# Performance work log

Measured on AMD Instinct MI355X. Metric: run time of the kernel, lower is better.

Reference implementation:

```python
import jax, jax.numpy as jnp
import numpy as np

IMG = 128      # raster_settings.image_size
FOCAL = 1.5    # simple pinhole projection (camera transform)
EPS = 1e-8
B, V, F = 4, 600, 1000


def setup_inputs() -> dict:
    key = jax.random.key(0)
    k1, k2 = jax.random.split(key)
    u = jax.random.uniform(k1, (B, V, 3), dtype=jnp.float32)
    xy = u[..., :2] * 2.0 - 1.0          # x,y in [-1, 1]
    z = u[..., 2:3] * 2.0 + 1.0          # z in [1, 3] (in front of camera)
    verts = jnp.concatenate([xy, z], axis=-1)   # [B, V, 3] world coords
    faces = jax.random.randint(k2, (F, 3), 0, V)  # [F, 3] vertex indices
    return {"verts": verts, "faces": faces}


def _pix_grid(H, W):
    # PyTorch3D NDC convention: +X left, +Y up; pixel centers at (2i+1)/S - 1 flipped.
    xs = 1.0 - (2.0 * jnp.arange(W, dtype=jnp.float32) + 1.0) / W
    ys = 1.0 - (2.0 * jnp.arange(H, dtype=jnp.float32) + 1.0) / H
    px = jnp.broadcast_to(xs[None, :], (H, W)).reshape(-1)  # [P]
    py = jnp.broadcast_to(ys[:, None], (H, W)).reshape(-1)  # [P]
    return px, py


def _edge(ax, ay, bx, by, px, py):
    # signed (twice-)area of triangle (a, b, p)
    return (bx - ax) * (py - ay) - (by - ay) * (px - ax)


def _seg_dist2(px, py, ax, ay, bx, by):
    # squared distance from point p to segment (a, b); all args broadcastable
    ex, ey = bx - ax, by - ay
    dx, dy = px - ax, py - ay
    ee = jnp.maximum(ex * ex + ey * ey, EPS)
    t = jnp.clip((dx * ex + dy * ey) / ee, 0.0, 1.0)
    rx = dx - t * ex
    ry = dy - t * ey
    return rx * rx + ry * ry


def _rasterize_one(v_ndc, faces, H, W):
    fv = v_ndc[faces]                       # [F, 3, 3] face vertices (ndc x, y, view z)
    v0, v1, v2 = fv[:, 0], fv[:, 1], fv[:, 2]
    px, py = _pix_grid(H, W)                # [P], P = H*W
    pxr, pyr = px[None, :], py[None, :]
    # signed face area [F]
    area = _edge(v0[:, 0], v0[:, 1], v1[:, 0], v1[:, 1], v2[:, 0], v2[:, 1])
    # edge functions at every pixel -> unnormalized barycentrics [F, P]
    w0 = _edge(v1[:, 0:1], v1[:, 1:2], v2[:, 0:1], v2[:, 1:2], pxr, pyr)
    w1 = _edge(v2[:, 0:1], v2[:, 1:2], v0[:, 0:1], v0[:, 1:2], pxr, pyr)
    w2 = _edge(v0[:, 0:1], v0[:, 1:2], v1[:, 0:1], v1[:, 1:2], pxr, pyr)
    denom = jnp.where(jnp.abs(area) > EPS, area, EPS)[:, None]
    s0, s1, s2 = w0 / denom, w1 / denom, w2 / denom
    zpix = s0 * v0[:, 2:3] + s1 * v1[:, 2:3] + s2 * v2[:, 2:3]  # [F, P]
    inside = (s0 >= 0) & (s1 >= 0) & (s2 >= 0) \
             & (jnp.abs(area)[:, None] > EPS) & (zpix > 0)
    zcand = jnp.where(inside, zpix, jnp.inf)
    idx = jnp.argmin(zcand, axis=0)                       # [P] winning face per pixel
    gather = lambda a: jnp.take_along_axis(a, idx[None, :], axis=0)[0]
    zmin = gather(zcand)
    hit = jnp.isfinite(zmin)
    b0, b1, b2 = gather(s0), gather(s1), gather(s2)       # winner barycentrics [P]
    # signed squared point-triangle distance at the winning face (negative inside)
    fw = fv[idx]                                          # [P, 3, 3]
    a, b, c = fw[:, 0], fw[:, 1], fw[:, 2]
    d2 = jnp.minimum(
        jnp.minimum(_seg_dist2(px, py, a[:, 0], a[:, 1], b[:, 0], b[:, 1]),
                    _seg_dist2(px, py, b[:, 0], b[:, 1], c[:, 0], c[:, 1])),
        _seg_dist2(px, py, c[:, 0], c[:, 1], a[:, 0], a[:, 1]))
    pix_to_face = jnp.where(hit, idx, -1).reshape(H, W)
    zbuf = jnp.where(hit, zmin, -1.0).reshape(H, W)
    bary = jnp.where(hit[:, None], jnp.stack([b0, b1, b2], -1), -1.0).reshape(H, W, 3)
    dists = jnp.where(hit, -d2, -1.0).reshape(H, W)
    return pix_to_face, zbuf, bary, dists


def reference(verts, faces):
    # camera transform: identity world-to-view, perspective projection, keep view z
    x = FOCAL * verts[..., 0] / verts[..., 2]
    y = FOCAL * verts[..., 1] / verts[..., 2]
    v_ndc = jnp.stack([x, y, verts[..., 2]], axis=-1)     # [B, V, 3]
    rast = lambda v: _rasterize_one(v, faces, IMG, IMG)
    pix_to_face, zbuf, bary, dists = jax.vmap(rast)(v_ndc)
    return pix_to_face, zbuf, bary, dists
```

## Files before the change

kernel.cpp:

```cpp
#include <hip/hip_runtime.h>
#include <math.h>

namespace {

constexpr int IMG  = 128;
constexpr int NPIX = IMG * IMG;
constexpr int B    = 4;
constexpr int V    = 600;
constexpr int F    = 1000;
constexpr float FOCALF = 1.5f;
constexpr float EPSF   = 1e-8f;
constexpr float SLACK  = 1e-5f;
constexpr float ZEPS    = 1e-4f;
constexpr float DENSAFE = 1e-3f;

__device__ inline float seg_dist2(float px, float py, float ax, float ay,
                                  float bx, float by) {
#pragma clang fp contract(off)
    float ex = bx - ax, ey = by - ay;
    float dx = px - ax, dy = py - ay;
    float ee = fmaxf(ex * ex + ey * ey, EPSF);
    float t  = (dx * ex + dy * ey) / ee;
    t = fminf(fmaxf(t, 0.0f), 1.0f);
    float rx = dx - t * ex;
    float ry = dy - t * ey;
    return rx * rx + ry * ry;
}

__global__ __launch_bounds__(256) void setup_clear(const float* __restrict__ verts,
                                                   const int* __restrict__ faces,
                                                   float* __restrict__ fdata,
                                                   unsigned long long* __restrict__ zbest) {
#pragma clang fp contract(off)
    int t = blockIdx.x * 256 + threadIdx.x;
    zbest[t] = ~0ULL;
    if (t >= B * F) return;
    int b = t / F, f = t - b * F;
    int i0 = faces[f * 3 + 0], i1 = faces[f * 3 + 1], i2 = faces[f * 3 + 2];
    const float* vb = verts + (size_t)b * V * 3;
    float x0 = vb[i0 * 3], y0 = vb[i0 * 3 + 1], z0 = vb[i0 * 3 + 2];
    float x1 = vb[i1 * 3], y1 = vb[i1 * 3 + 1], z1 = vb[i1 * 3 + 2];
    float x2 = vb[i2 * 3], y2 = vb[i2 * 3 + 1], z2 = vb[i2 * 3 + 2];
    float ax = (FOCALF * x0) / z0, ay = (FOCALF * y0) / z0;
    float bx = (FOCALF * x1) / z1, by = (FOCALF * y1) / z1;
    float cx = (FOCALF * x2) / z2, cy = (FOCALF * y2) / z2;
    float e0x = cx - bx, e0y = cy - by;
    float e1x = ax - cx, e1y = ay - cy;
    float e2x = bx - ax, e2y = by - ay;
    float den = e2x * (cy - ay) - e2y * (cx - ax);
    if (!(fabsf(den) > EPSF)) den = 0.0f;
    float* o = fdata + ((size_t)t << 4);
    o[0]  = e0x; o[1]  = e0y; o[2]  = bx;  o[3]  = by;
    o[4]  = e1x; o[5]  = e1y; o[6]  = cx;  o[7]  = cy;
    o[8]  = e2x; o[9]  = e2y; o[10] = ax;  o[11] = ay;
    o[12] = den; o[13] = z0;  o[14] = z1;  o[15] = z2;
}

__global__ __launch_bounds__(512, 8) void rast(const float* __restrict__ fdata,
                                               unsigned long long* __restrict__ zbest) {
#pragma clang fp contract(off)
    __shared__ float4 sface[64 * 4];
    __shared__ unsigned int lticket;
    const int tid  = threadIdx.x;
    const int lane = tid & 63;
    const int bk   = blockIdx.x;
    const int ch   = bk & 15;
    const int b    = (bk >> 4) & 3;
    const int slice = bk >> 6;
    if (tid == 0) lticket = 0u;

    const int f0 = ch * 64;
    const int sz = min(64, F - f0);
    const int fl = min(f0 + lane, F - 1);
    const float4* fd4 = (const float4*)(fdata + (((size_t)b * F + fl) << 4));
    const float4 q0 = fd4[0], q1 = fd4[1], q2 = fd4[2], q3 = fd4[3];
    if (tid < 64) {
        sface[tid * 4 + 0] = q0;
        sface[tid * 4 + 1] = q1;
        sface[tid * 4 + 2] = q2;
        sface[tid * 4 + 3] = q3;
    }
    __syncthreads();

    const bool valid = (lane < sz) & (q3.x != 0.0f);
    const float s = q3.x > 0.0f ? 1.0f : -1.0f;
    const float g0x = s * q0.x, g0y = s * q0.y;
    const float g1x = s * q1.x, g1y = s * q1.y;
    const float g2x = s * q2.x, g2y = s * q2.y;
    const bool c0y = g0x >= 0.0f, c0x = g0y >= 0.0f;
    const bool c1y = g1x >= 0.0f, c1x = g1y >= 0.0f;
    const bool c2y = g2x >= 0.0f, c2x = g2y >= 0.0f;

    const int dpx = lane & 7, dpy = lane >> 3;

    for (;;) {
        unsigned int j = 0;
        if (lane == 0) j = atomicAdd(&lticket, 1u);
        j = (unsigned int)__shfl((int)j, 0);
        if (j >= 16u) break;
        const unsigned int jj = (j + (unsigned int)ch) & 15u;

        const int row = (slice >> 2) + 4 * (int)(jj >> 2);
        const int col = (slice & 3) + 4 * (int)(jj & 3);
        const int ix0 = col * 8, iy0 = row * 8;
        const int ix  = ix0 + dpx, iy = iy0 + dpy;
        const float px = 1.0f - (2.0f * (float)ix + 1.0f) / (float)IMG;
        const float py = 1.0f - (2.0f * (float)iy + 1.0f) / (float)IMG;
        const float pxmax = 1.0f - (2.0f * (float)ix0 + 1.0f) / (float)IMG;
        const float pxmin = 1.0f - (2.0f * (float)(ix0 + 7) + 1.0f) / (float)IMG;
        const float pymax = 1.0f - (2.0f * (float)iy0 + 1.0f) / (float)IMG;
        const float pymin = 1.0f - (2.0f * (float)(iy0 + 7) + 1.0f) / (float)IMG;

        const int gp = b * NPIX + iy * IMG + ix;
        const unsigned ztop = (unsigned)(zbest[gp] >> 32);
        float zbf  = (ztop == 0xFFFFFFFFu) ? INFINITY : __uint_as_float(ztop);
        float zbfp = zbf + ZEPS;

        bool pass = valid;
        pass &= (g0x * ((c0y ? pymax : pymin) - q0.w)
               - g0y * ((c0x ? pxmin : pxmax) - q0.z)) >= -SLACK;
        pass &= (g1x * ((c1y ? pymax : pymin) - q1.w)
               - g1y * ((c1x ? pxmin : pxmax) - q1.z)) >= -SLACK;
        pass &= (g2x * ((c2y ? pymax : pymin) - q2.w)
               - g2y * ((c2x ? pxmin : pxmax) - q2.z)) >= -SLACK;

        unsigned long long pmin = ~0ULL;
        unsigned long long mask = __ballot(pass);
        while (mask) {
            const int sl = __builtin_ctzll(mask);
            mask &= mask - 1;
            const float4 r0 = sface[sl * 4 + 0];
            const float4 r1 = sface[sl * 4 + 1];
            const float4 r2 = sface[sl * 4 + 2];
            const float4 r3 = sface[sl * 4 + 3];
            const float den = r3.x;
            float w0 = r0.x * (py - r0.w) - r0.y * (px - r0.z);
            float w1 = r1.x * (py - r1.w) - r1.y * (px - r1.z);
            float w2 = r2.x * (py - r2.w) - r2.y * (px - r2.z);

            const bool i0 = !(w0 * den < 0.0f);
            const bool i1 = !(w1 * den < 0.0f);
            const bool i2 = !(w2 * den < 0.0f);
            const float rd  = __builtin_amdgcn_rcpf(den);
            const float zt  = (w0 * rd) * r3.y + (w1 * rd) * r3.z + (w2 * rd) * r3.w;
            const bool densmall = fabsf(den) < DENSAFE;
            const bool need = (i0 & i1 & i2) &
                              (densmall | ((zt < zbfp) & (zt > -ZEPS)));
            if (__any(need)) {
                const unsigned ds = __float_as_uint(den) >> 31;
                const bool in0 = (w0 == 0.0f) | ((__float_as_uint(w0) >> 31) == ds);
                const bool in1 = (w1 == 0.0f) | ((__float_as_uint(w1) >> 31) == ds);
                const bool in2 = (w2 == 0.0f) | ((__float_as_uint(w2) >> 31) == ds);
                if (in0 & in1 & in2) {
                    float s0 = w0 / den, s1 = w1 / den, s2 = w2 / den;
                    float z  = s0 * r3.y + s1 * r3.z + s2 * r3.w;
                    if (z > 0.0f) {
                        unsigned long long pk =
                            ((unsigned long long)__float_as_uint(z) << 32) |
                            (unsigned)(f0 + sl);
                        pmin = pmin < pk ? pmin : pk;
                        zbf  = fminf(zbf, z);
                        zbfp = zbf + ZEPS;
                    }
                }
            }
        }
        if (pmin != ~0ULL) atomicMin(&zbest[gp], pmin);
    }
}

__global__ __launch_bounds__(256) void pass2(const float* __restrict__ fdata,
                                             const unsigned long long* __restrict__ zbest,
                                             float* __restrict__ out) {
#pragma clang fp contract(off)
    const int gp = blockIdx.x * 256 + threadIdx.x;
    const int b  = gp >> 14;
    const int p  = gp & (NPIX - 1);
    const int ix = p & (IMG - 1), iy = p >> 7;

    unsigned long long packed = zbest[gp];
    float o_face = -1.0f, o_z = -1.0f, o_b0 = -1.0f, o_b1 = -1.0f,
          o_b2 = -1.0f, o_d = -1.0f;

    if (packed != ~0ULL) {
        const int   idx = (int)(unsigned)(packed & 0xffffffffu);
        const float z   = __uint_as_float((unsigned)(packed >> 32));
        const float px  = 1.0f - (2.0f * (float)ix + 1.0f) / (float)IMG;
        const float py  = 1.0f - (2.0f * (float)iy + 1.0f) / (float)IMG;

        const float4* fd4 = (const float4*)(fdata + (((size_t)b * F + idx) << 4));
        float4 q0 = fd4[0], q1 = fd4[1], q2 = fd4[2], q3 = fd4[3];
        float den = q3.x;
        float w0 = q0.x * (py - q0.w) - q0.y * (px - q0.z);
        float w1 = q1.x * (py - q1.w) - q1.y * (px - q1.z);
        float w2 = q2.x * (py - q2.w) - q2.y * (px - q2.z);
        float s0 = w0 / den, s1 = w1 / den, s2 = w2 / den;

        float d2 = fminf(fminf(seg_dist2(px, py, q2.z, q2.w, q0.z, q0.w),
                               seg_dist2(px, py, q0.z, q0.w, q1.z, q1.w)),
                         seg_dist2(px, py, q1.z, q1.w, q2.z, q2.w));
        o_face = (float)idx; o_z = z;
        o_b0 = s0; o_b1 = s1; o_b2 = s2;
        o_d = -d2;
    }

    out[gp]            = o_face;
    out[B * NPIX + gp] = o_z;
    const int bary_base = 2 * B * NPIX;
    out[bary_base + gp * 3 + 0] = o_b0;
    out[bary_base + gp * 3 + 1] = o_b1;
    out[bary_base + gp * 3 + 2] = o_b2;
    out[5 * B * NPIX + gp] = o_d;
}

}

extern "C" void kernel_launch(void* const* d_in, const int* in_sizes, int n_in,
                              void* d_out, int out_size, void* d_ws, size_t ws_size,
                              hipStream_t stream) {
    const float* verts = (const float*)d_in[0];
    const int*   faces = (const int*)d_in[1];
    float* out = (float*)d_out;

    char* ws = (char*)d_ws;
    unsigned long long* zbest = (unsigned long long*)ws;
    float* fdata = (float*)(ws + (size_t)B * NPIX * 8);

    setup_clear<<<B * NPIX / 256, 256, 0, stream>>>(verts, faces, fdata, zbest);
    rast<<<1024, 512, 0, stream>>>(fdata, zbest);
    pass2<<<B * NPIX / 256, 256, 0, stream>>>(fdata, zbest, out);
}
```

Before: 31.78 us.

## Precompute normalized edge-function planes and z-plane for cheaper per-face culling

The face setup now precomputes sign-normalized edge equations (a*x+b*y+c), a barycentric sum constant, a linear depth plane, and a per-face depth tolerance. Face records grow from 16 to 28 floats and are padded to 1024 faces per batch, with degenerate or padding faces marked dead. The inner loop first runs a cheap two-FMA edge test with a wave-level early exit, then a planar depth test, and only loads the exact edge data for candidates. This cuts per-candidate ALU and LDS traffic in the hot loop, at the cost of more setup work and memory per face, plus new epsilon tolerances that could affect exactness.

```diff
diff --git a/kernel.cpp b/kernel.cpp
--- a/kernel.cpp
+++ b/kernel.cpp
@@ -8,10 +8,11 @@
 constexpr int B    = 4;
 constexpr int V    = 600;
 constexpr int F    = 1000;
+constexpr int FP   = 1024;
 constexpr float FOCALF = 1.5f;
 constexpr float EPSF   = 1e-8f;
-constexpr float SLACK  = 1e-5f;
-constexpr float ZEPS    = 1e-4f;
+constexpr float EW   = 1e-4f;
+constexpr float EBIN = 2e-4f;
 constexpr float DENSAFE = 1e-3f;
 
 __device__ inline float seg_dist2(float px, float py, float ax, float ay,
@@ -34,32 +35,59 @@
 #pragma clang fp contract(off)
     int t = blockIdx.x * 256 + threadIdx.x;
     zbest[t] = ~0ULL;
-    if (t >= B * F) return;
-    int b = t / F, f = t - b * F;
-    int i0 = faces[f * 3 + 0], i1 = faces[f * 3 + 1], i2 = faces[f * 3 + 2];
-    const float* vb = verts + (size_t)b * V * 3;
-    float x0 = vb[i0 * 3], y0 = vb[i0 * 3 + 1], z0 = vb[i0 * 3 + 2];
-    float x1 = vb[i1 * 3], y1 = vb[i1 * 3 + 1], z1 = vb[i1 * 3 + 2];
-    float x2 = vb[i2 * 3], y2 = vb[i2 * 3 + 1], z2 = vb[i2 * 3 + 2];
-    float ax = (FOCALF * x0) / z0, ay = (FOCALF * y0) / z0;
-    float bx = (FOCALF * x1) / z1, by = (FOCALF * y1) / z1;
-    float cx = (FOCALF * x2) / z2, cy = (FOCALF * y2) / z2;
-    float e0x = cx - bx, e0y = cy - by;
-    float e1x = ax - cx, e1y = ay - cy;
-    float e2x = bx - ax, e2y = by - ay;
-    float den = e2x * (cy - ay) - e2y * (cx - ax);
-    if (!(fabsf(den) > EPSF)) den = 0.0f;
-    float* o = fdata + ((size_t)t << 4);
-    o[0]  = e0x; o[1]  = e0y; o[2]  = bx;  o[3]  = by;
-    o[4]  = e1x; o[5]  = e1y; o[6]  = cx;  o[7]  = cy;
-    o[8]  = e2x; o[9]  = e2y; o[10] = ax;  o[11] = ay;
-    o[12] = den; o[13] = z0;  o[14] = z1;  o[15] = z2;
+    if (t >= B * FP) return;
+    const int b = t >> 10, fp = t & (FP - 1);
+    float* o = fdata + (size_t)t * 28;
+    bool dead = (fp >= F);
+    float e0x=0,e0y=0,bx=0,by=0,e1x=0,e1y=0,cx=0,cy=0,e2x=0,e2y=0,ax=0,ay=0;
+    float den=0, z0=0, z1=0, z2=0;
+    if (!dead) {
+        int i0 = faces[fp * 3 + 0], i1 = faces[fp * 3 + 1], i2 = faces[fp * 3 + 2];
+        const float* vb = verts + (size_t)b * V * 3;
+        float x0 = vb[i0 * 3], y0 = vb[i0 * 3 + 1]; z0 = vb[i0 * 3 + 2];
+        float x1 = vb[i1 * 3], y1 = vb[i1 * 3 + 1]; z1 = vb[i1 * 3 + 2];
+        float x2 = vb[i2 * 3], y2 = vb[i2 * 3 + 1]; z2 = vb[i2 * 3 + 2];
+        ax = (FOCALF * x0) / z0; ay = (FOCALF * y0) / z0;
+        bx = (FOCALF * x1) / z1; by = (FOCALF * y1) / z1;
+        cx = (FOCALF * x2) / z2; cy = (FOCALF * y2) / z2;
+        e0x = cx - bx; e0y = cy - by;
+        e1x = ax - cx; e1y = ay - cy;
+        e2x = bx - ax; e2y = by - ay;
+        den = e2x * (cy - ay) - e2y * (cx - ax);
+        if (!(fabsf(den) > EPSF)) { den = 0.0f; dead = true; }
+    }
+    if (dead) {
+        o[0] = 0.0f; o[1] = 0.0f; o[2] = -1e30f; o[3] = 0.0f;
+        #pragma unroll
+        for (int k = 4; k < 28; ++k) o[k] = 0.0f;
+        return;
+    }
+    float a0 = -e0y, b0 = e0x, c0 = e0y * bx - e0x * by;
+    float a1 = -e1y, b1 = e1x, c1 = e1y * cx - e1x * cy;
+    float a2 = -e2y, b2 = e2x, c2 = e2y * ax - e2x * ay;
+    const float s  = den > 0.0f ? 1.0f : -1.0f;
+    const float rd = __builtin_amdgcn_rcpf(den);
+    const float azr = z0 * rd, bzr = z1 * rd, czr = z2 * rd;
+    const float Zx = a0 * azr + a1 * bzr + a2 * czr;
+    const float Zy = b0 * azr + b1 * bzr + b2 * czr;
+    const float Zc = c0 * azr + c1 * bzr + c2 * czr;
+    const float S = (fabsf(a0) + fabsf(b0) + fabsf(c0)) * fabsf(azr)
+                  + (fabsf(a1) + fabsf(b1) + fabsf(c1)) * fabsf(bzr)
+                  + (fabsf(a2) + fabsf(b2) + fabsf(c2)) * fabsf(czr);
+    const float eps = (fabsf(den) < DENSAFE) ? INFINITY : (1e-4f + 2e-6f * S);
+    o[0]  = s * a0; o[1]  = s * b0; o[2]  = s * c0; o[3]  = s * den;
+    o[4]  = s * a1; o[5]  = s * b1; o[6]  = s * c1; o[7]  = eps;
+    o[8]  = Zx;     o[9]  = Zy;     o[10] = Zc;     o[11] = 0.0f;
+    o[12] = e0x;    o[13] = e0y;    o[14] = bx;     o[15] = by;
+    o[16] = e1x;    o[17] = e1y;    o[18] = cx;     o[19] = cy;
+    o[20] = e2x;    o[21] = e2y;    o[22] = ax;     o[23] = ay;
+    o[24] = den;    o[25] = z0;     o[26] = z1;     o[27] = z2;
 }
 
 __global__ __launch_bounds__(512, 8) void rast(const float* __restrict__ fdata,
                                                unsigned long long* __restrict__ zbest) {
 #pragma clang fp contract(off)
-    __shared__ float4 sface[64 * 4];
+    __shared__ float4 sface[64 * 7];
     __shared__ unsigned int lticket;
     const int tid  = threadIdx.x;
     const int lane = tid & 63;
@@ -70,26 +98,18 @@
     if (tid == 0) lticket = 0u;
 
     const int f0 = ch * 64;
-    const int sz = min(64, F - f0);
-    const int fl = min(f0 + lane, F - 1);
-    const float4* fd4 = (const float4*)(fdata + (((size_t)b * F + fl) << 4));
-    const float4 q0 = fd4[0], q1 = fd4[1], q2 = fd4[2], q3 = fd4[3];
-    if (tid < 64) {
-        sface[tid * 4 + 0] = q0;
-        sface[tid * 4 + 1] = q1;
-        sface[tid * 4 + 2] = q2;
-        sface[tid * 4 + 3] = q3;
-    }
+    const float4* gflat = (const float4*)(fdata + (size_t)(b * FP + f0) * 28);
+    if (tid < 448) ((float4*)sface)[tid] = gflat[tid];
+
+    const float4* fd4 = (const float4*)(fdata + (size_t)(b * FP + f0 + lane) * 28);
+    const float4 m0 = fd4[0], m1 = fd4[1];
+    const float a2s = -(m0.x + m1.x);
+    const float b2s = -(m0.y + m1.y);
+    const float c2s = m0.w - m0.z - m1.z;
+    const bool c0x = m0.x >= 0.0f, c0y = m0.y >= 0.0f;
+    const bool c1x = m1.x >= 0.0f, c1y = m1.y >= 0.0f;
+    const bool c2x = a2s >= 0.0f, c2y = b2s >= 0.0f;
     __syncthreads();
-
-    const bool valid = (lane < sz) & (q3.x != 0.0f);
-    const float s = q3.x > 0.0f ? 1.0f : -1.0f;
-    const float g0x = s * q0.x, g0y = s * q0.y;
-    const float g1x = s * q1.x, g1y = s * q1.y;
-    const float g2x = s * q2.x, g2y = s * q2.y;
-    const bool c0y = g0x >= 0.0f, c0x = g0y >= 0.0f;
-    const bool c1y = g1x >= 0.0f, c1x = g1y >= 0.0f;
-    const bool c2y = g2x >= 0.0f, c2x = g2y >= 0.0f;
 
     const int dpx = lane & 7, dpy = lane >> 3;
 
@@ -113,40 +133,42 @@
 
         const int gp = b * NPIX + iy * IMG + ix;
         const unsigned ztop = (unsigned)(zbest[gp] >> 32);
-        float zbf  = (ztop == 0xFFFFFFFFu) ? INFINITY : __uint_as_float(ztop);
-        float zbfp = zbf + ZEPS;
-
-        bool pass = valid;
-        pass &= (g0x * ((c0y ? pymax : pymin) - q0.w)
-               - g0y * ((c0x ? pxmin : pxmax) - q0.z)) >= -SLACK;
-        pass &= (g1x * ((c1y ? pymax : pymin) - q1.w)
-               - g1y * ((c1x ? pxmin : pxmax) - q1.z)) >= -SLACK;
-        pass &= (g2x * ((c2y ? pymax : pymin) - q2.w)
-               - g2y * ((c2x ? pxmin : pxmax) - q2.z)) >= -SLACK;
+        float zbf = (ztop == 0xFFFFFFFFu) ? INFINITY : __uint_as_float(ztop);
+
+        bool pass =
+            (m0.x * (c0x ? pxmax : pxmin) + m0.y * (c0y ? pymax : pymin) + m0.z)
+                >= -EBIN;
+        pass &=
+            (m1.x * (c1x ? pxmax : pxmin) + m1.y * (c1y ? pymax : pymin) + m1.z)
+                >= -EBIN;
+        pass &=
+            (a2s * (c2x ? pxmax : pxmin) + b2s * (c2y ? pymax : pymin) + c2s)
+                >= -EBIN;
 
         unsigned long long pmin = ~0ULL;
         unsigned long long mask = __ballot(pass);
         while (mask) {
             const int sl = __builtin_ctzll(mask);
             mask &= mask - 1;
-            const float4 r0 = sface[sl * 4 + 0];
-            const float4 r1 = sface[sl * 4 + 1];
-            const float4 r2 = sface[sl * 4 + 2];
-            const float4 r3 = sface[sl * 4 + 3];
-            const float den = r3.x;
-            float w0 = r0.x * (py - r0.w) - r0.y * (px - r0.z);
-            float w1 = r1.x * (py - r1.w) - r1.y * (px - r1.z);
-            float w2 = r2.x * (py - r2.w) - r2.y * (px - r2.z);
-
-            const bool i0 = !(w0 * den < 0.0f);
-            const bool i1 = !(w1 * den < 0.0f);
-            const bool i2 = !(w2 * den < 0.0f);
-            const float rd  = __builtin_amdgcn_rcpf(den);
-            const float zt  = (w0 * rd) * r3.y + (w1 * rd) * r3.z + (w2 * rd) * r3.w;
-            const bool densmall = fabsf(den) < DENSAFE;
-            const bool need = (i0 & i1 & i2) &
-                              (densmall | ((zt < zbfp) & (zt > -ZEPS)));
+            const float4 k0 = sface[sl * 7 + 0];
+            const float4 k1 = sface[sl * 7 + 1];
+            const float g0 = fmaf(k0.x, px, fmaf(k0.y, py, k0.z));
+            const float g1 = fmaf(k1.x, px, fmaf(k1.y, py, k1.z));
+            const float g2 = k0.w - g0 - g1;
+            const bool maybe = (g0 >= -EW) & (g1 >= -EW) & (g2 >= -EW);
+            if (!__any(maybe)) continue;
+            const float4 kz = sface[sl * 7 + 2];
+            const float zt = fmaf(kz.x, px, fmaf(kz.y, py, kz.z));
+            const bool need = maybe & (zt < zbf + k1.w);
             if (__any(need)) {
+                const float4 r0 = sface[sl * 7 + 3];
+                const float4 r1 = sface[sl * 7 + 4];
+                const float4 r2 = sface[sl * 7 + 5];
+                const float4 r3 = sface[sl * 7 + 6];
+                const float den = r3.x;
+                float w0 = r0.x * (py - r0.w) - r0.y * (px - r0.z);
+                float w1 = r1.x * (py - r1.w) - r1.y * (px - r1.z);
+                float w2 = r2.x * (py - r2.w) - r2.y * (px - r2.z);
                 const unsigned ds = __float_as_uint(den) >> 31;
                 const bool in0 = (w0 == 0.0f) | ((__float_as_uint(w0) >> 31) == ds);
                 const bool in1 = (w1 == 0.0f) | ((__float_as_uint(w1) >> 31) == ds);
@@ -160,7 +182,6 @@
                             (unsigned)(f0 + sl);
                         pmin = pmin < pk ? pmin : pk;
                         zbf  = fminf(zbf, z);
-                        zbfp = zbf + ZEPS;
                     }
                 }
             }
@@ -188,8 +209,8 @@
         const float px  = 1.0f - (2.0f * (float)ix + 1.0f) / (float)IMG;
         const float py  = 1.0f - (2.0f * (float)iy + 1.0f) / (float)IMG;
 
-        const float4* fd4 = (const float4*)(fdata + (((size_t)b * F + idx) << 4));
-        float4 q0 = fd4[0], q1 = fd4[1], q2 = fd4[2], q3 = fd4[3];
+        const float4* fd4 = (const float4*)(fdata + (size_t)(b * FP + idx) * 28);
+        float4 q0 = fd4[3], q1 = fd4[4], q2 = fd4[5], q3 = fd4[6];
         float den = q3.x;
         float w0 = q0.x * (py - q0.w) - q0.y * (px - q0.z);
         float w1 = q1.x * (py - q1.w) - q1.y * (px - q1.z);
```

Result: no change. 31.42 us (-1.1%).
